# Kernel optimization log

Measured on AMD Instinct MI355X. Metric: run time of the kernel, lower is better.

## Reference

```python
import jax, jax.numpy as jnp
import numpy as np

HEADS = 8
DIM_HEAD = 64
QLEVEL = 127.0  # symmetric int8: clamp to [-128, 127]


def fake_quant(x):
    """Symmetric per-tensor int8 fake quantization with straight-through estimator."""
    delta = jnp.max(jnp.abs(x)) / QLEVEL
    xq = jnp.clip(jnp.round(x / delta), -128.0, 127.0) * delta
    return x + jax.lax.stop_gradient(xq - x)


def setup_inputs() -> dict:
    key = jax.random.key(0)
    ks = jax.random.split(key, 7)
    b, n, m, d, dc = 2, 4096, 1024, 512, 768
    return {
        "x": jax.random.normal(ks[0], (b, n, d), jnp.float32),
        "context": jax.random.normal(ks[1], (b, m, dc), jnp.float32),
        "Wq": jax.random.normal(ks[2], (d, d), jnp.float32) * 0.02,
        "Wk": jax.random.normal(ks[3], (dc, d), jnp.float32) * 0.02,
        "Wv": jax.random.normal(ks[4], (dc, d), jnp.float32) * 0.02,
        "Wo": jax.random.normal(ks[5], (d, d), jnp.float32) * 0.02,
        "bo": jnp.zeros((d,), jnp.float32),
    }


def reference(x, context, Wq, Wk, Wv, Wo, bo):
    b, n, _ = x.shape
    h, dh = HEADS, DIM_HEAD
    scale = dh ** -0.5

    q = x @ Wq            # [b, n, h*dh]
    k = context @ Wk      # [b, m, h*dh]
    v = context @ Wv      # [b, m, h*dh]

    def split(t):  # b n (h d) -> b h n d
        return t.reshape(t.shape[0], t.shape[1], h, dh).transpose(0, 2, 1, 3)

    q, k, v = split(q), split(k), split(v)

    # fake-quantize q and k before the score matmul (use_aq=True path)
    q = fake_quant(q)
    k = fake_quant(k)
    sim = jnp.einsum('bhid,bhjd->bhij', q, k) * scale  # [b, h, n, m]
    attn = jax.nn.softmax(sim, axis=-1)

    # fake-quantize attention weights and v before the AV matmul
    out = jnp.einsum('bhij,bhjd->bhid', fake_quant(attn), fake_quant(v))
    out = out.transpose(0, 2, 1, 3).reshape(b, n, h * dh)  # b h n d -> b n (h d)
    return out @ Wo + bo  # to_out[0]; to_out[-1] is Dropout (identity in eval)
```

## Files before the change

### kernel.cpp

```cpp
#include <hip/hip_runtime.h>
#include <stdint.h>

typedef float  v4f  __attribute__((ext_vector_type(4)));
typedef int    v4i  __attribute__((ext_vector_type(4)));
typedef __bf16 v8bf __attribute__((ext_vector_type(8)));
typedef __bf16 v4bf __attribute__((ext_vector_type(4)));

#define BATCH  2
#define NQ     4096
#define MK     1024
#define DMODEL 512
#define DCTX   768
#define NH     8
#define DH     64

__global__ __launch_bounds__(256) void k_prep(
    const float* __restrict__ x, const float* __restrict__ ctx,
    __bf16* __restrict__ xb, __bf16* __restrict__ cb,
    const float* __restrict__ Wq, const float* __restrict__ Wk,
    const float* __restrict__ Wv, const float* __restrict__ Wo,
    __bf16* __restrict__ Wq_t, __bf16* __restrict__ Wk_t,
    __bf16* __restrict__ Wv_t, __bf16* __restrict__ Wo_t,
    unsigned* __restrict__ scal) {
  int bx = blockIdx.x;
  if (bx < 2816) {
    const int XC = BATCH * NQ * DMODEL / 8;
    const int CC = BATCH * MK * DCTX / 8;
    int idx = bx * 256 + threadIdx.x;
    const float* src; __bf16* dst;
    if (idx < XC) { src = x + (size_t)idx * 8; dst = xb + (size_t)idx * 8; }
    else {
      int j = idx - XC;
      if (j >= CC) return;
      src = ctx + (size_t)j * 8; dst = cb + (size_t)j * 8;
    }
    float4 a = *(const float4*)src, b = *(const float4*)(src + 4);
    v8bf o = { (__bf16)a.x, (__bf16)a.y, (__bf16)a.z, (__bf16)a.w,
               (__bf16)b.x, (__bf16)b.y, (__bf16)b.z, (__bf16)b.w };
    *(v8bf*)dst = o;
    return;
  }
  int id = bx - 2816;
  if (id == 0 && threadIdx.x < 4) scal[threadIdx.x] = 0u;
  int tx = id & 15, rem = id >> 4;
  int ty = rem % 24, tz = rem / 24;
  const float* src; __bf16* dst; int K;
  switch (tz) {
    case 0:  src = Wq; dst = Wq_t; K = DMODEL; break;
    case 1:  src = Wk; dst = Wk_t; K = DCTX;   break;
    case 2:  src = Wv; dst = Wv_t; K = DCTX;   break;
    default: src = Wo; dst = Wo_t; K = DMODEL; break;
  }
  int k0 = ty * 32;
  if (k0 >= K) return;
  int n0 = tx * 32;
  __shared__ __bf16 tile[32][33];
  int c = threadIdx.x & 31, r0 = threadIdx.x >> 5;
  for (int i = 0; i < 4; ++i) {
    int r = r0 + i * 8;
    tile[c][r] = (__bf16)src[(size_t)(k0 + r) * DMODEL + n0 + c];
  }
  __syncthreads();
  for (int i = 0; i < 4; ++i) {
    int r = r0 + i * 8;
    dst[(size_t)(n0 + r) * K + k0 + c] = tile[r][c];
  }
}

template<int K_, int NC, bool BIAS, bool AMAX>
__device__ __forceinline__ void gemm_body(
    char* smemraw, const __bf16* __restrict__ A, const __bf16* __restrict__ Bt,
    float* __restrict__ C, int N, int rowBlk, int colBlk,
    const float* __restrict__ bias,
    unsigned* __restrict__ amaxLo, unsigned* __restrict__ amaxHi) {
  constexpr int CS = K_ + 8;
  constexpr int GPC = K_ / 8;
  constexpr int JT = NC / 16;
  constexpr int NIT = K_ / 32;
  constexpr int AD = 4;
  constexpr int AF = 4;
  __bf16* Bs = (__bf16*)smemraw;
  float* redmax = (float*)(smemraw + (size_t)NC * CS * 2);
  const int tid = threadIdx.x;
  const int lane = tid & 63, wave = tid >> 6;
  const int l15 = lane & 15, g = lane >> 4;
  const int col0 = colBlk * NC;
  const int row0w = rowBlk * 256 + wave * 64;

#pragma unroll
  for (int i = 0; i < NC * GPC / 256; ++i) {
    int f = i * 256 + tid;
    int c = f / GPC, w = f - c * GPC;
    *(v8bf*)(&Bs[c * CS + w * 8]) =
        *(const v8bf*)(Bt + (size_t)(col0 + c) * K_ + w * 8);
  }

  const __bf16* ap[AF];
#pragma unroll
  for (int f = 0; f < AF; ++f)
    ap[f] = A + (size_t)(row0w + f * 16 + l15) * K_ + g * 8;

  v8bf abuf[AF][AD];
#pragma unroll
  for (int i = 0; i < AD; ++i)
#pragma unroll
    for (int f = 0; f < AF; ++f)
      abuf[f][i] = *(const v8bf*)(ap[f] + i * 32);
  __syncthreads();

  v8bf bbuf[2][JT];
#pragma unroll
  for (int j = 0; j < JT; ++j)
    bbuf[0][j] = *(const v8bf*)(&Bs[(j * 16 + l15) * CS + g * 8]);

  v4f acc[AF][JT] = {};
#pragma unroll
  for (int it = 0; it < NIT; ++it) {
    const int cur = it & 1, nxt = cur ^ 1;
    if (it + 1 < NIT) {
#pragma unroll
      for (int j = 0; j < JT; ++j)
        bbuf[nxt][j] =
            *(const v8bf*)(&Bs[(j * 16 + l15) * CS + (it + 1) * 32 + g * 8]);
    }
    v8bf af[AF];
#pragma unroll
    for (int f = 0; f < AF; ++f) {
      af[f] = abuf[f][it % AD];
      if (it + AD < NIT)
        abuf[f][it % AD] = *(const v8bf*)(ap[f] + (it + AD) * 32);
    }
#pragma unroll
    for (int f = 0; f < AF; ++f)
#pragma unroll
      for (int j = 0; j < JT; ++j)
        acc[f][j] = __builtin_amdgcn_mfma_f32_16x16x32_bf16(
            af[f], bbuf[cur][j], acc[f][j], 0, 0, 0);
  }

  float lmax = 0.0f;
#pragma unroll
  for (int j = 0; j < JT; ++j) {
    int col = col0 + j * 16 + l15;
    float bv = BIAS ? bias[col] : 0.0f;
#pragma unroll
    for (int f = 0; f < AF; ++f) {
#pragma unroll
      for (int r = 0; r < 4; ++r) {
        int row = row0w + f * 16 + g * 4 + r;
        float cv = acc[f][j][r] + bv;
        C[(size_t)row * N + col] = cv;
        if (AMAX) lmax = fmaxf(lmax, fabsf(cv));
      }
    }
  }
  if (AMAX) {
    for (int off = 32; off > 0; off >>= 1)
      lmax = fmaxf(lmax, __shfl_xor(lmax, off, 64));
    if (lane == 0) redmax[wave] = lmax;
    __syncthreads();
    if (tid == 0) {
      float bm = fmaxf(fmaxf(redmax[0], redmax[1]), fmaxf(redmax[2], redmax[3]));
      atomicMax(col0 < 512 ? amaxLo : amaxHi, __float_as_uint(bm));
    }
  }
}

__global__ __launch_bounds__(256, 2) void k_gemm_qkv(
    const __bf16* __restrict__ xb, const __bf16* __restrict__ Wq_t,
    float* __restrict__ qf,
    const __bf16* __restrict__ cb, const __bf16* __restrict__ Wkv_t,
    float* __restrict__ kvf, unsigned* __restrict__ scal) {
  __shared__ __align__(16) char smem[64 * (512 + 8) * 2 + 16];
  int bid = blockIdx.x;
  if (bid < 256) {
    int xcd = bid & 7, w = bid >> 3;
    gemm_body<512, 64, false, true>(smem, xb, Wq_t, qf, 512,
                                    xcd * 4 + (w >> 3), w & 7, nullptr,
                                    scal + 0, scal + 0);
  } else {
    int id = bid - 256;
    int xcd = id & 7, w = id >> 3;
    gemm_body<768, 32, false, true>(smem, cb, Wkv_t, kvf, 1024,
                                    xcd, w, nullptr,
                                    scal + 1, scal + 2);
  }
}

__global__ __launch_bounds__(256, 2) void k_gemm_out(
    const __bf16* __restrict__ o, const __bf16* __restrict__ Wo_t,
    float* __restrict__ out, const float* __restrict__ bo) {
  __shared__ __align__(16) char smem[64 * (512 + 8) * 2 + 16];
  int xcd = blockIdx.x & 7, w = blockIdx.x >> 3;
  gemm_body<512, 64, true, false>(smem, o, Wo_t, out, 512,
                                  xcd * 4 + (w >> 3), w & 7, bo,
                                  nullptr, nullptr);
}

__global__ __launch_bounds__(256) void k_quant_kv(
    const float* __restrict__ kvf,
    int8_t* __restrict__ k8, int8_t* __restrict__ v8t,
    const unsigned* __restrict__ scal) {
  __shared__ int8_t tile[64][80];
  int bx = blockIdx.x;
  if (bx < 1024) {
    int j = bx * 256 + threadIdx.x;
    int r = j >> 7;
    int c4 = (j & 127) << 2;
    float4 v = *(const float4*)(kvf + (size_t)r * 1024 + c4);
    float s = 127.0f / __uint_as_float(scal[1]);
    int a0 = __float2int_rn(v.x * s), a1 = __float2int_rn(v.y * s);
    int a2 = __float2int_rn(v.z * s), a3 = __float2int_rn(v.w * s);
    a0 = max(-128, min(127, a0)); a1 = max(-128, min(127, a1));
    a2 = max(-128, min(127, a2)); a3 = max(-128, min(127, a3));
    unsigned p = (unsigned)(a0 & 255) | ((unsigned)(a1 & 255) << 8) |
                 ((unsigned)(a2 & 255) << 16) | ((unsigned)(a3 & 255) << 24);
    *(unsigned*)(k8 + (size_t)j * 4) = p;
    return;
  }
  int id = bx - 1024;
  int bh = id >> 4, b = bh >> 3, h = bh & 7;
  int j0 = (id & 15) * 64;
  const float s = 127.0f / __uint_as_float(scal[2]);
  int t = threadIdx.x;
  int j = t >> 2, dh0 = (t & 3) << 4;
  const float* src = kvf + (size_t)(b * MK + j0 + j) * 1024 + 512 + h * DH + dh0;
#pragma unroll
  for (int i = 0; i < 16; i += 4) {
    float4 v = *(const float4*)(src + i);
    int a0 = __float2int_rn(v.x * s), a1 = __float2int_rn(v.y * s);
    int a2 = __float2int_rn(v.z * s), a3 = __float2int_rn(v.w * s);
    tile[dh0 + i + 0][j] = (int8_t)max(-128, min(127, a0));
    tile[dh0 + i + 1][j] = (int8_t)max(-128, min(127, a1));
    tile[dh0 + i + 2][j] = (int8_t)max(-128, min(127, a2));
    tile[dh0 + i + 3][j] = (int8_t)max(-128, min(127, a3));
  }
  __syncthreads();
  int dh = t >> 2, jb = (t & 3) << 4;
  v4i val = *(const v4i*)(&tile[dh][jb]);
  *(v4i*)(v8t + (size_t)(bh * DH + dh) * MK + j0 + jb) = val;
}

__device__ __forceinline__ v4i quant_pack16(const float* p, float s) {
  v4i out;
#pragma unroll
  for (int q = 0; q < 4; ++q) {
    float4 v = *(const float4*)(p + q * 4);
    int a0 = __float2int_rn(v.x * s), a1 = __float2int_rn(v.y * s);
    int a2 = __float2int_rn(v.z * s), a3 = __float2int_rn(v.w * s);
    a0 = max(-128, min(127, a0)); a1 = max(-128, min(127, a1));
    a2 = max(-128, min(127, a2)); a3 = max(-128, min(127, a3));
    out[q] = (int)((unsigned)(a0 & 255) | ((unsigned)(a1 & 255) << 8) |
                   ((unsigned)(a2 & 255) << 16) | ((unsigned)(a3 & 255) << 24));
  }
  return out;
}

__global__ __launch_bounds__(256, 4) void k_pass1(
    const float* __restrict__ qf, int8_t* __restrict__ q8,
    const int8_t* __restrict__ k8,
    float* __restrict__ invz, unsigned* __restrict__ scal) {
  __shared__ __align__(16) int8_t kbuf[128 * 72];
  __shared__ float mared[4];
  int bh = blockIdx.y, b = bh >> 3, h = bh & 7;
  int wave = threadIdx.x >> 6, lane = threadIdx.x & 63;
  int l15 = lane & 15, g = lane >> 4;
  int row0 = blockIdx.x * 64;
  int myrow = row0 + wave * 16 + l15;
  const float aq = __uint_as_float(scal[0]), ak = __uint_as_float(scal[1]);
  const float alpha2 = (aq * ak) * (0.125f / (127.0f * 127.0f)) * 1.44269504f;
  const float sq = 127.0f / aq;
  const v4i z4 = {0, 0, 0, 0};
  size_t qoff = (size_t)(b * NQ + myrow) * DMODEL + h * DH + g * 16;
  v4i qfrag = quant_pack16(qf + qoff, sq);
  *(v4i*)(q8 + qoff) = qfrag;
  const int8_t* kbase = k8 + (size_t)b * MK * DMODEL + h * DH;
  const int rs = threadIdx.x >> 2, qs = (threadIdx.x & 3) * 16;
  const int8_t* kls = kbase + (size_t)rs * DMODEL + qs;

  v4i kp0 = *(const v4i*)(kls);
  v4i kp1 = *(const v4i*)(kls + (size_t)64 * DMODEL);

  float z[4] = {0.f, 0.f, 0.f, 0.f};
  int mi = -(1 << 30);
  for (int tile = 0; tile < 8; ++tile) {
    __syncthreads();
    *(v4i*)(&kbuf[rs * 72 + qs]) = kp0;
    *(v4i*)(&kbuf[(rs + 64) * 72 + qs]) = kp1;
    __syncthreads();
    if (tile < 7) {
      kp0 = *(const v4i*)(kls + (size_t)((tile + 1) * 128) * DMODEL);
      kp1 = *(const v4i*)(kls + (size_t)((tile + 1) * 128 + 64) * DMODEL);
    }
    float zt = z[tile >> 1];
#pragma unroll
    for (int t = 0; t < 8; ++t) {
      v4i kfrag = *(const v4i*)(&kbuf[(t * 16 + l15) * 72 + g * 16]);
      v4i sa = __builtin_amdgcn_mfma_i32_16x16x64_i8(kfrag, qfrag, z4, 0, 0, 0);
      mi = max(mi, max(max(sa[0], sa[1]), max(sa[2], sa[3])));
      float e0 = __builtin_amdgcn_exp2f((float)sa[0] * alpha2);
      float e1 = __builtin_amdgcn_exp2f((float)sa[1] * alpha2);
      float e2 = __builtin_amdgcn_exp2f((float)sa[2] * alpha2);
      float e3 = __builtin_amdgcn_exp2f((float)sa[3] * alpha2);
      zt += (e0 + e1) + (e2 + e3);
    }
    z[tile >> 1] = zt;
  }
#pragma unroll
  for (int i = 0; i < 4; ++i) {
    z[i] += __shfl_xor(z[i], 16, 64);
    z[i] += __shfl_xor(z[i], 32, 64);
  }
  mi = max(mi, __shfl_xor(mi, 16, 64));
  mi = max(mi, __shfl_xor(mi, 32, 64));
  float zt = (z[0] + z[1]) + (z[2] + z[3]);
  float iz = 1.0f / zt;
  if (g == 0) invz[(size_t)bh * NQ + myrow] = iz;
  float ma = __builtin_amdgcn_exp2f((float)mi * alpha2) * iz;
#pragma unroll
  for (int off = 1; off < 16; off <<= 1)
    ma = fmaxf(ma, __shfl_xor(ma, off, 64));
  if (lane == 0) mared[wave] = ma;
  __syncthreads();
  if (threadIdx.x == 0)
    atomicMax(scal + 3,
              __float_as_uint(fmaxf(fmaxf(mared[0], mared[1]),
                                    fmaxf(mared[2], mared[3]))));
}

__global__ __launch_bounds__(256, 4) void k_pass2(
    const int8_t* __restrict__ q8, const int8_t* __restrict__ k8,
    const int8_t* __restrict__ v8t, const float* __restrict__ invz,
    const unsigned* __restrict__ scal, __bf16* __restrict__ o) {
  __shared__ __align__(16) int8_t kbuf[128 * 72];
  __shared__ __align__(16) int8_t vbuf[64 * 152];
  __shared__ __align__(16) int8_t albuf[4][16 * 152];
  int bh = blockIdx.y, b = bh >> 3, h = bh & 7;
  int wave = threadIdx.x >> 6, lane = threadIdx.x & 63;
  int l15 = lane & 15, g = lane >> 4;
  int row0 = blockIdx.x * 64;
  int myrow = row0 + wave * 16 + l15;
  const float aq = __uint_as_float(scal[0]), ak = __uint_as_float(scal[1]);
  const float avv = __uint_as_float(scal[2]), izm = __uint_as_float(scal[3]);
  const float alpha2 = (aq * ak) * (0.125f / (127.0f * 127.0f)) * 1.44269504f;
  const float oscale = (izm / 127.0f) * (avv / 127.0f);
  const float MAGIC = 12582912.0f;
  const v4i z4 = {0, 0, 0, 0};

  v4i qfrag = *(const v4i*)(q8 + (size_t)(b * NQ + myrow) * DMODEL + h * DH + g * 16);
  const float lcr = __builtin_amdgcn_logf(invz[(size_t)bh * NQ + myrow] * (127.0f / izm));
  const int8_t* kbase = k8 + (size_t)b * MK * DMODEL + h * DH;
  const int8_t* vbase = v8t + (size_t)bh * DH * MK;
  int8_t* alds = albuf[wave];
  const int rs = threadIdx.x >> 2, qs = (threadIdx.x & 3) * 16;
  const int vr = threadIdx.x >> 3, vq = (threadIdx.x & 7) * 16;
  const int8_t* kls = kbase + (size_t)rs * DMODEL + qs;
  const int8_t* vls = vbase + (size_t)vr * MK + vq;

  v4i kp0 = *(const v4i*)(kls);
  v4i kp1 = *(const v4i*)(kls + (size_t)64 * DMODEL);
  v4i vp0 = *(const v4i*)(vls);
  v4i vp1 = *(const v4i*)(vls + (size_t)32 * MK);

  v4i pacc[4] = {};
  for (int tile = 0; tile < 8; ++tile) {
    __syncthreads();
    *(v4i*)(&kbuf[rs * 72 + qs]) = kp0;
    *(v4i*)(&kbuf[(rs + 64) * 72 + qs]) = kp1;
    *(v4i*)(&vbuf[vr * 152 + vq]) = vp0;
    *(v4i*)(&vbuf[(vr + 32) * 152 + vq]) = vp1;
    __syncthreads();
    if (tile < 7) {
      kp0 = *(const v4i*)(kls + (size_t)((tile + 1) * 128) * DMODEL);
      kp1 = *(const v4i*)(kls + (size_t)((tile + 1) * 128 + 64) * DMODEL);
      vp0 = *(const v4i*)(vls + (tile + 1) * 128);
      vp1 = *(const v4i*)(vls + (size_t)32 * MK + (tile + 1) * 128);
    }
#pragma unroll
    for (int t = 0; t < 8; ++t) {
      v4i kfrag = *(const v4i*)(&kbuf[(t * 16 + l15) * 72 + g * 16]);
      v4i sa = __builtin_amdgcn_mfma_i32_16x16x64_i8(kfrag, qfrag, z4, 0, 0, 0);
      float f0 = __builtin_amdgcn_exp2f(fmaf((float)sa[0], alpha2, lcr)) + MAGIC;
      float f1 = __builtin_amdgcn_exp2f(fmaf((float)sa[1], alpha2, lcr)) + MAGIC;
      float f2 = __builtin_amdgcn_exp2f(fmaf((float)sa[2], alpha2, lcr)) + MAGIC;
      float f3 = __builtin_amdgcn_exp2f(fmaf((float)sa[3], alpha2, lcr)) + MAGIC;
      unsigned packed = (__float_as_uint(f0) & 255u) |
                        ((__float_as_uint(f1) & 255u) << 8) |
                        ((__float_as_uint(f2) & 255u) << 16) |
                        (__float_as_uint(f3) << 24);
      *(unsigned*)(alds + l15 * 152 + t * 16 + g * 4) = packed;
    }
#pragma unroll
    for (int c = 0; c < 2; ++c) {
      v4i afrag = *(const v4i*)(alds + l15 * 152 + c * 64 + g * 16);
#pragma unroll
      for (int d = 0; d < 4; ++d) {
        v4i vfrag = *(const v4i*)(&vbuf[(d * 16 + l15) * 152 + c * 64 + g * 16]);
        pacc[d] = __builtin_amdgcn_mfma_i32_16x16x64_i8(vfrag, afrag, pacc[d], 0, 0, 0);
      }
    }
  }
  __bf16* obase = o + (size_t)(b * NQ + row0 + wave * 16 + l15) * DMODEL + h * DH;
#pragma unroll
  for (int d = 0; d < 4; ++d) {
    v4bf ov;
#pragma unroll
    for (int r = 0; r < 4; ++r)
      ov[r] = (__bf16)((float)pacc[d][r] * oscale);
    *(v4bf*)(obase + d * 16 + g * 4) = ov;
  }
}

extern "C" void kernel_launch(void* const* d_in, const int* in_sizes, int n_in,
                              void* d_out, int out_size, void* d_ws, size_t ws_size,
                              hipStream_t stream) {
  (void)in_sizes; (void)n_in; (void)out_size; (void)ws_size;
  const float* x   = (const float*)d_in[0];
  const float* ctx = (const float*)d_in[1];
  const float* Wq  = (const float*)d_in[2];
  const float* Wk  = (const float*)d_in[3];
  const float* Wv  = (const float*)d_in[4];
  const float* Wo  = (const float*)d_in[5];
  const float* bo  = (const float*)d_in[6];
  float* out = (float*)d_out;

  char* ws = (char*)d_ws;
  size_t off = 0;
  auto alloc = [&](size_t bytes) {
    char* p = ws + off;
    off += (bytes + 255) & ~(size_t)255;
    return p;
  };
  unsigned* scal = (unsigned*)alloc(16);
  __bf16* Wq_t = (__bf16*)alloc((size_t)512 * 512 * 2);
  __bf16* Wk_t = (__bf16*)alloc((size_t)512 * 768 * 2);
  __bf16* Wv_t = (__bf16*)alloc((size_t)512 * 768 * 2);
  __bf16* Wo_t = (__bf16*)alloc((size_t)512 * 512 * 2);
  __bf16* xb   = (__bf16*)alloc((size_t)BATCH * NQ * DMODEL * 2);
  __bf16* cb   = (__bf16*)alloc((size_t)BATCH * MK * DCTX * 2);
  float* qf  = (float*)alloc((size_t)BATCH * NQ * DMODEL * 4);
  float* kvf = (float*)alloc((size_t)BATCH * MK * 1024 * 4);
  int8_t* q8 = (int8_t*)alloc((size_t)BATCH * NQ * DMODEL);
  int8_t* k8 = (int8_t*)alloc((size_t)BATCH * MK * DMODEL);
  int8_t* v8t = (int8_t*)alloc((size_t)BATCH * NH * DH * MK);
  float* invz = (float*)alloc((size_t)BATCH * NH * NQ * 4);
  __bf16* o = (__bf16*)qf;

  k_prep<<<4352, 256, 0, stream>>>(x, ctx, xb, cb, Wq, Wk, Wv, Wo,
                                   Wq_t, Wk_t, Wv_t, Wo_t, scal);
  k_gemm_qkv<<<512, 256, 0, stream>>>(xb, Wq_t, qf, cb, Wk_t, kvf, scal);
  k_quant_kv<<<1280, 256, 0, stream>>>(kvf, k8, v8t, scal);
  k_pass1<<<dim3(64, 16), 256, 0, stream>>>(qf, q8, k8, invz, scal);
  k_pass2<<<dim3(64, 16), 256, 0, stream>>>(q8, k8, v8t, invz, scal, o);
  k_gemm_out<<<256, 256, 0, stream>>>(o, Wo_t, out, bo);
}
```

Before: 175.6 us.

## Double-buffer K/V LDS tiles and transpose attention fragments via cross-lane shuffles

```diff
diff --git a/kernel.cpp b/kernel.cpp
--- a/kernel.cpp
+++ b/kernel.cpp
@@ -260,7 +260,7 @@
     const float* __restrict__ qf, int8_t* __restrict__ q8,
     const int8_t* __restrict__ k8,
     float* __restrict__ invz, unsigned* __restrict__ scal) {
-  __shared__ __align__(16) int8_t kbuf[128 * 72];
+  __shared__ __align__(16) int8_t kbuf[2][128 * 72];
   __shared__ float mared[4];
   int bh = blockIdx.y, b = bh >> 3, h = bh & 7;
   int wave = threadIdx.x >> 6, lane = threadIdx.x & 63;
@@ -280,13 +280,13 @@
 
   v4i kp0 = *(const v4i*)(kls);
   v4i kp1 = *(const v4i*)(kls + (size_t)64 * DMODEL);
+  *(v4i*)(&kbuf[0][rs * 72 + qs]) = kp0;
+  *(v4i*)(&kbuf[0][(rs + 64) * 72 + qs]) = kp1;
 
   float z[4] = {0.f, 0.f, 0.f, 0.f};
   int mi = -(1 << 30);
   for (int tile = 0; tile < 8; ++tile) {
-    __syncthreads();
-    *(v4i*)(&kbuf[rs * 72 + qs]) = kp0;
-    *(v4i*)(&kbuf[(rs + 64) * 72 + qs]) = kp1;
+    const int cur = tile & 1;
     __syncthreads();
     if (tile < 7) {
       kp0 = *(const v4i*)(kls + (size_t)((tile + 1) * 128) * DMODEL);
@@ -295,7 +295,7 @@
     float zt = z[tile >> 1];
 #pragma unroll
     for (int t = 0; t < 8; ++t) {
-      v4i kfrag = *(const v4i*)(&kbuf[(t * 16 + l15) * 72 + g * 16]);
+      v4i kfrag = *(const v4i*)(&kbuf[cur][(t * 16 + l15) * 72 + g * 16]);
       v4i sa = __builtin_amdgcn_mfma_i32_16x16x64_i8(kfrag, qfrag, z4, 0, 0, 0);
       mi = max(mi, max(max(sa[0], sa[1]), max(sa[2], sa[3])));
       float e0 = __builtin_amdgcn_exp2f((float)sa[0] * alpha2);
@@ -305,6 +305,10 @@
       zt += (e0 + e1) + (e2 + e3);
     }
     z[tile >> 1] = zt;
+    if (tile < 7) {
+      *(v4i*)(&kbuf[cur ^ 1][rs * 72 + qs]) = kp0;
+      *(v4i*)(&kbuf[cur ^ 1][(rs + 64) * 72 + qs]) = kp1;
+    }
   }
 #pragma unroll
   for (int i = 0; i < 4; ++i) {
@@ -332,9 +336,8 @@
     const int8_t* __restrict__ q8, const int8_t* __restrict__ k8,
     const int8_t* __restrict__ v8t, const float* __restrict__ invz,
     const unsigned* __restrict__ scal, __bf16* __restrict__ o) {
-  __shared__ __align__(16) int8_t kbuf[128 * 72];
-  __shared__ __align__(16) int8_t vbuf[64 * 152];
-  __shared__ __align__(16) int8_t albuf[4][16 * 152];
+  __shared__ __align__(16) int8_t kbuf[2][128 * 72];
+  __shared__ __align__(16) int8_t vbuf[2][64 * 152];
   int bh = blockIdx.y, b = bh >> 3, h = bh & 7;
   int wave = threadIdx.x >> 6, lane = threadIdx.x & 63;
   int l15 = lane & 15, g = lane >> 4;
@@ -351,7 +354,6 @@
   const float lcr = __builtin_amdgcn_logf(invz[(size_t)bh * NQ + myrow] * (127.0f / izm));
   const int8_t* kbase = k8 + (size_t)b * MK * DMODEL + h * DH;
   const int8_t* vbase = v8t + (size_t)bh * DH * MK;
-  int8_t* alds = albuf[wave];
   const int rs = threadIdx.x >> 2, qs = (threadIdx.x & 3) * 16;
   const int vr = threadIdx.x >> 3, vq = (threadIdx.x & 7) * 16;
   const int8_t* kls = kbase + (size_t)rs * DMODEL + qs;
@@ -361,14 +363,14 @@
   v4i kp1 = *(const v4i*)(kls + (size_t)64 * DMODEL);
   v4i vp0 = *(const v4i*)(vls);
   v4i vp1 = *(const v4i*)(vls + (size_t)32 * MK);
+  *(v4i*)(&kbuf[0][rs * 72 + qs]) = kp0;
+  *(v4i*)(&kbuf[0][(rs + 64) * 72 + qs]) = kp1;
+  *(v4i*)(&vbuf[0][vr * 152 + vq]) = vp0;
+  *(v4i*)(&vbuf[0][(vr + 32) * 152 + vq]) = vp1;
 
   v4i pacc[4] = {};
   for (int tile = 0; tile < 8; ++tile) {
-    __syncthreads();
-    *(v4i*)(&kbuf[rs * 72 + qs]) = kp0;
-    *(v4i*)(&kbuf[(rs + 64) * 72 + qs]) = kp1;
-    *(v4i*)(&vbuf[vr * 152 + vq]) = vp0;
-    *(v4i*)(&vbuf[(vr + 32) * 152 + vq]) = vp1;
+    const int cur = tile & 1;
     __syncthreads();
     if (tile < 7) {
       kp0 = *(const v4i*)(kls + (size_t)((tile + 1) * 128) * DMODEL);
@@ -376,28 +378,52 @@
       vp0 = *(const v4i*)(vls + (tile + 1) * 128);
       vp1 = *(const v4i*)(vls + (size_t)32 * MK + (tile + 1) * 128);
     }
+    int w[8];
 #pragma unroll
     for (int t = 0; t < 8; ++t) {
-      v4i kfrag = *(const v4i*)(&kbuf[(t * 16 + l15) * 72 + g * 16]);
+      v4i kfrag = *(const v4i*)(&kbuf[cur][(t * 16 + l15) * 72 + g * 16]);
       v4i sa = __builtin_amdgcn_mfma_i32_16x16x64_i8(kfrag, qfrag, z4, 0, 0, 0);
       float f0 = __builtin_amdgcn_exp2f(fmaf((float)sa[0], alpha2, lcr)) + MAGIC;
       float f1 = __builtin_amdgcn_exp2f(fmaf((float)sa[1], alpha2, lcr)) + MAGIC;
       float f2 = __builtin_amdgcn_exp2f(fmaf((float)sa[2], alpha2, lcr)) + MAGIC;
       float f3 = __builtin_amdgcn_exp2f(fmaf((float)sa[3], alpha2, lcr)) + MAGIC;
-      unsigned packed = (__float_as_uint(f0) & 255u) |
-                        ((__float_as_uint(f1) & 255u) << 8) |
-                        ((__float_as_uint(f2) & 255u) << 16) |
-                        (__float_as_uint(f3) << 24);
-      *(unsigned*)(alds + l15 * 152 + t * 16 + g * 4) = packed;
+      w[t] = (int)((__float_as_uint(f0) & 255u) |
+                   ((__float_as_uint(f1) & 255u) << 8) |
+                   ((__float_as_uint(f2) & 255u) << 16) |
+                   (__float_as_uint(f3) << 24));
     }
 #pragma unroll
     for (int c = 0; c < 2; ++c) {
-      v4i afrag = *(const v4i*)(alds + l15 * 152 + c * 64 + g * 16);
+      int wc0 = w[c * 4 + 0], wc1 = w[c * 4 + 1];
+      int wc2 = w[c * 4 + 2], wc3 = w[c * 4 + 3];
+      int t0 = (g & 1) ? wc0 : wc1;
+      int r0 = __shfl_xor(t0, 16, 64);
+      int t1 = (g & 1) ? wc2 : wc3;
+      int r1 = __shfl_xor(t1, 16, 64);
+      int a0 = (g & 1) ? r0 : wc0;
+      int a1 = (g & 1) ? wc1 : r0;
+      int a2 = (g & 1) ? r1 : wc2;
+      int a3 = (g & 1) ? wc3 : r1;
+      int u0 = (g & 2) ? a0 : a2;
+      int s0 = __shfl_xor(u0, 32, 64);
+      int u1 = (g & 2) ? a1 : a3;
+      int s1 = __shfl_xor(u1, 32, 64);
+      v4i afrag;
+      afrag[0] = (g & 2) ? s0 : a0;
+      afrag[1] = (g & 2) ? s1 : a1;
+      afrag[2] = (g & 2) ? a2 : s0;
+      afrag[3] = (g & 2) ? a3 : s1;
 #pragma unroll
       for (int d = 0; d < 4; ++d) {
-        v4i vfrag = *(const v4i*)(&vbuf[(d * 16 + l15) * 152 + c * 64 + g * 16]);
+        v4i vfrag = *(const v4i*)(&vbuf[cur][(d * 16 + l15) * 152 + c * 64 + g * 16]);
         pacc[d] = __builtin_amdgcn_mfma_i32_16x16x64_i8(vfrag, afrag, pacc[d], 0, 0, 0);
       }
+    }
+    if (tile < 7) {
+      *(v4i*)(&kbuf[cur ^ 1][rs * 72 + qs]) = kp0;
+      *(v4i*)(&kbuf[cur ^ 1][(rs + 64) * 72 + qs]) = kp1;
+      *(v4i*)(&vbuf[cur ^ 1][vr * 152 + vq]) = vp0;
+      *(v4i*)(&vbuf[cur ^ 1][(vr + 32) * 152 + vq]) = vp1;
     }
   }
   __bf16* obase = o + (size_t)(b * NQ + row0 + wave * 16 + l15) * DMODEL + h * DH;
```

Result: faster. 170.2 us (median of 2 runs) (-3.1%).
